# Kernel optimization log

Measured on AMD Instinct MI355X. Metric: run time of the kernel, lower is better.

## Reference

```python
import jax, jax.numpy as jnp
import numpy as np

CORE_DIM = 128
MEMORY_SLOTS = 64
B, S = 4, 4096


def setup_inputs() -> dict:
    key = jax.random.key(0)
    k1, k2, k3, k4, k5 = jax.random.split(key, 5)
    x = jax.random.normal(k1, (B, S, CORE_DIM), dtype=jnp.float32)
    memory_keys = jax.random.normal(k2, (MEMORY_SLOTS, CORE_DIM), dtype=jnp.float32)
    memory_ops = jax.random.normal(k3, (MEMORY_SLOTS, CORE_DIM, CORE_DIM), dtype=jnp.float32)
    # nn.Linear(core_dim, core_dim): weight [out, in], bias [out]
    bound = 1.0 / np.sqrt(CORE_DIM)
    Wq = jax.random.uniform(k4, (CORE_DIM, CORE_DIM), minval=-bound, maxval=bound, dtype=jnp.float32)
    bq = jax.random.uniform(k5, (CORE_DIM,), minval=-bound, maxval=bound, dtype=jnp.float32)
    return {"input_tensor": x, "memory_keys": memory_keys, "memory_ops": memory_ops, "Wq": Wq, "bq": bq}


def reference(input_tensor, memory_keys, memory_ops, Wq, bq):
    dim = input_tensor.shape[-1]
    # query projection: x @ Wq^T + bq
    queries = jnp.einsum('bsd,ed->bse', input_tensor, Wq) + bq
    # soft attention over memory slots
    attn_logits = jnp.einsum('bsd,md->bsm', queries, memory_keys)
    attn_weights = jax.nn.softmax(attn_logits / jnp.sqrt(jnp.float32(dim)), axis=-1)
    # fused: (sum_m attn[bsm] * ops[m]) @ x[bs]  == sum_m attn[bsm] * (ops[m] @ x[bs])
    processed = jnp.einsum('bsm,mde,bse->bsd', attn_weights, memory_ops, input_tensor)
    return processed
```

## Files before the change

kernel.cpp:

```cpp
#include <hip/hip_runtime.h>

typedef __bf16 bf16x8 __attribute__((ext_vector_type(8)));
typedef float f32x4 __attribute__((ext_vector_type(4)));
typedef unsigned int uint4v __attribute__((ext_vector_type(4)));
typedef unsigned short ushort_t;
typedef unsigned int uint_t;

#define RS 0.08838834764831845f

__device__ __forceinline__ ushort_t f2bf(float f) {
    uint_t u = __float_as_uint(f);
    u += 0x7FFFu + ((u >> 16) & 1u);
    return (ushort_t)(u >> 16);
}
__device__ __forceinline__ uint_t pack2(float a, float b) {
    return (uint_t)f2bf(a) | ((uint_t)f2bf(b) << 16);
}
union U4B8 { uint4v u; bf16x8 b; };
__device__ __forceinline__ bf16x8 as_bf(uint4v u) { U4B8 x; x.u = u; return x.b; }

__device__ __forceinline__ int xfrag(int f, int lane) {
    return f * 1072 + ((lane >> 4) * 272) + ((lane & 15) * 16);
}

__device__ __forceinline__ void gload16(const void* g, void* l) {
    __builtin_amdgcn_global_load_lds(
        (const __attribute__((address_space(1))) void*)g,
        (__attribute__((address_space(3))) void*)l, 16, 0, 0);
}

__global__ __launch_bounds__(256) void prep_kernel(
    const float* __restrict__ ops, const float* __restrict__ keys,
    const float* __restrict__ Wq, const float* __restrict__ bq,
    uint4v* __restrict__ ops_sw, ushort_t* __restrict__ kp_sw,
    float* __restrict__ cb)
{
    const int tid = threadIdx.x;
    const int b = blockIdx.x;
    if (b >= 64) {
        int g = (b - 64) * 256 + tid;
        int L = g & 63, dt = (g >> 6) & 7, ks = (g >> 9) & 3, m = g >> 11;
        int d = dt * 16 + (L & 15);
        int e0 = ks * 32 + ((L >> 4) << 3);
        const float4* s = (const float4*)(ops + (((size_t)(m * 128 + d)) << 7) + e0);
        float4 v0 = s[0], v1 = s[1];
        uint4v o = { pack2(v0.x, v0.y), pack2(v0.z, v0.w),
                     pack2(v1.x, v1.y), pack2(v1.z, v1.w) };
        int h = m * 2048 + (dt >> 2) * 1024 + ks * 256 + (dt & 3) * 64 + L;
        ops_sw[h] = o;
    } else {
        __shared__ float red[256];
        const int m = b;
        const int d = tid & 127, eh = tid >> 7;
        const float* kr = keys + m * 128 + eh * 64;
        const float* wc = Wq + (size_t)(eh * 64) * 128 + d;
        float acc = 0.f;
        #pragma unroll 8
        for (int e = 0; e < 64; ++e)
            acc = fmaf(kr[e], wc[(size_t)e * 128], acc);
        red[tid] = acc;
        __syncthreads();
        if (tid < 128) {
            float v = red[tid] + red[tid + 128];
            int ki = d >> 5, qq = (d >> 3) & 3, j = d & 7;
            kp_sw[((((ki * 4 + (m >> 4)) * 64) + (qq * 16 + (m & 15))) << 3) | j] = f2bf(v);
        } else if (tid >= 192) {
            int lane = tid - 192;
            float p = keys[m * 128 + lane] * bq[lane]
                    + keys[m * 128 + 64 + lane] * bq[64 + lane];
            #pragma unroll
            for (int off = 1; off < 64; off <<= 1) p += __shfl_xor(p, off);
            if (lane == 0) cb[m] = p;
        }
    }
}

__global__ __launch_bounds__(512, 2) void main_kernel(
    const float* __restrict__ x, const float* __restrict__ cb,
    const ushort_t* __restrict__ kp_sw, const uint4v* __restrict__ ops_sw,
    float* __restrict__ out)
{
    __shared__ __align__(16) unsigned char lds[132096];
    float* attn_f = (float*)lds;
    unsigned char* xs = lds + 33792;
    uint4v* bb = (uint4v*)(lds + 33792);

    const int tid = threadIdx.x;
    const int lane = tid & 63;
    const int w = tid >> 6;
    const int q = lane >> 4;
    const int l15 = lane & 15;
    const int tb = blockIdx.x >> 1;
    const int dh = blockIdx.x & 1;
    const int t0 = tb * 128;
    const int dtp = w & 3;
    const int tg = w >> 2;

    {
        const float4* x4 = (const float4*)(x + (size_t)t0 * 128);
        #pragma unroll
        for (int it = 0; it < 4; ++it) {
            int i = it * 512 + tid;
            int t = i >> 4, kc = i & 15;
            float4 a = x4[t * 32 + kc * 2];
            float4 b2 = x4[t * 32 + kc * 2 + 1];
            uint4v o = { pack2(a.x, a.y), pack2(a.z, a.w),
                         pack2(b2.x, b2.y), pack2(b2.z, b2.w) };
            *(uint4v*)(xs + ((t >> 4) * 4 + (kc >> 2)) * 1072
                          + (kc & 3) * 272 + (t & 15) * 16) = o;
        }
    }
    __syncthreads();

    {
        f32x4 L0 = {0,0,0,0}, L1 = {0,0,0,0}, L2 = {0,0,0,0}, L3 = {0,0,0,0};
        const uint4v* kpf = (const uint4v*)kp_sw;
        #pragma unroll
        for (int ki = 0; ki < 4; ++ki) {
            bf16x8 a = *(const bf16x8*)(xs + xfrag(w * 4 + ki, lane));
            L0 = __builtin_amdgcn_mfma_f32_16x16x32_bf16(a, as_bf(kpf[(ki*4+0)*64 + lane]), L0, 0,0,0);
            L1 = __builtin_amdgcn_mfma_f32_16x16x32_bf16(a, as_bf(kpf[(ki*4+1)*64 + lane]), L1, 0,0,0);
            L2 = __builtin_amdgcn_mfma_f32_16x16x32_bf16(a, as_bf(kpf[(ki*4+2)*64 + lane]), L2, 0,0,0);
            L3 = __builtin_amdgcn_mfma_f32_16x16x32_bf16(a, as_bf(kpf[(ki*4+3)*64 + lane]), L3, 0,0,0);
        }
        float c0 = cb[l15], c1 = cb[16 + l15], c2 = cb[32 + l15], c3 = cb[48 + l15];
        #pragma unroll
        for (int r = 0; r < 4; ++r) {
            float v0 = (L0[r] + c0) * RS;
            float v1 = (L1[r] + c1) * RS;
            float v2 = (L2[r] + c2) * RS;
            float v3 = (L3[r] + c3) * RS;
            float mx = fmaxf(fmaxf(v0, v1), fmaxf(v2, v3));
            #pragma unroll
            for (int off = 1; off < 16; off <<= 1) mx = fmaxf(mx, __shfl_xor(mx, off));
            float e0 = __expf(v0 - mx), e1 = __expf(v1 - mx),
                  e2 = __expf(v2 - mx), e3 = __expf(v3 - mx);
            float sm = e0 + e1 + e2 + e3;
            #pragma unroll
            for (int off = 1; off < 16; off <<= 1) sm += __shfl_xor(sm, off);
            float inv = 1.0f / sm;
            int t = w * 16 + q * 4 + r;
            attn_f[(     l15) * 132 + t] = e0 * inv;
            attn_f[(16 + l15) * 132 + t] = e1 * inv;
            attn_f[(32 + l15) * 132 + t] = e2 * inv;
            attn_f[(48 + l15) * 132 + t] = e3 * inv;
        }
    }

    bf16x8 A[4][4];
    #pragma unroll
    for (int tf = 0; tf < 4; ++tf)
        #pragma unroll
        for (int ki = 0; ki < 4; ++ki)
            A[tf][ki] = *(const bf16x8*)(xs + xfrag(tg * 16 + tf * 4 + ki, lane));

    __syncthreads();

    auto stage = [&](int pair, int b) {
        uint4v* dst = bb + b * 2048 + w * 64;
        const uint4v* src = ops_sw + (size_t)pair * 4096 + dh * 1024 + w * 64 + lane;
        #pragma unroll
        for (int j = 0; j < 4; ++j) {
            const uint4v* g = src + (j >> 1) * 2048 + (j & 1) * 512;
            gload16((const void*)g, (void*)(dst + j * 512));
        }
    };

    f32x4 C[4] = {};

    auto computePair = [&](int p) {
        const uint4v* bbuf = bb + (p % 3) * 2048 + dtp * 64 + lane;
        #pragma unroll
        for (int sl = 0; sl < 2; ++sl) {
            const int m = p * 2 + sl;
            f32x4 S[4] = {};
            __builtin_amdgcn_s_setprio(1);
            #pragma unroll
            for (int ki = 0; ki < 4; ++ki) {
                bf16x8 bfrag = as_bf(bbuf[sl * 1024 + ki * 256]);
                #pragma unroll
                for (int tf = 0; tf < 4; ++tf)
                    S[tf] = __builtin_amdgcn_mfma_f32_16x16x32_bf16(A[tf][ki], bfrag, S[tf], 0,0,0);
            }
            __builtin_amdgcn_s_setprio(0);
            #pragma unroll
            for (int tf = 0; tf < 4; ++tf) {
                f32x4 af = *(const f32x4*)&attn_f[m * 132 + tg * 64 + tf * 16 + q * 4];
                #pragma unroll
                for (int r = 0; r < 4; ++r)
                    C[tf][r] = fmaf(af[r], S[tf][r], C[tf][r]);
            }
        }
    };

    stage(0, 0);
    for (int p = 0; p < 31; ++p) {
        stage(p + 1, (p + 1) % 3);
        asm volatile("s_waitcnt vmcnt(4)" ::: "memory");
        __builtin_amdgcn_s_barrier();
        computePair(p);
    }
    asm volatile("s_waitcnt vmcnt(0)" ::: "memory");
    __builtin_amdgcn_s_barrier();
    computePair(31);

    float* op = out + (size_t)t0 * 128 + dh * 64 + dtp * 16 + l15;
    #pragma unroll
    for (int tf = 0; tf < 4; ++tf)
        #pragma unroll
        for (int r = 0; r < 4; ++r)
            op[(size_t)(tg * 64 + tf * 16 + q * 4 + r) * 128] = C[tf][r];
}

extern "C" void kernel_launch(void* const* d_in, const int* in_sizes, int n_in,
                              void* d_out, int out_size, void* d_ws, size_t ws_size,
                              hipStream_t stream)
{
    const float* x    = (const float*)d_in[0];
    const float* keys = (const float*)d_in[1];
    const float* ops  = (const float*)d_in[2];
    const float* Wq   = (const float*)d_in[3];
    const float* bq   = (const float*)d_in[4];
    float* out = (float*)d_out;

    char* ws = (char*)d_ws;
    uint4v*   ops_sw = (uint4v*)ws;
    ushort_t* kp_sw  = (ushort_t*)(ws + 2097152);
    float*    cb     = (float*)(ws + 2097152 + 16384);

    prep_kernel<<<576, 256, 0, stream>>>(ops, keys, Wq, bq, ops_sw, kp_sw, cb);
    main_kernel<<<256, 512, 0, stream>>>(x, cb, kp_sw, ops_sw, out);
}
```

Baseline: 104.7 us.

## Fuse prep into main kernel with a grid-wide atomic barrier

Merges the weight-preparation kernel into the main kernel. Every block converts its share of the memory ops to bf16, and the first 64 blocks compute the projected keys and bias terms. A device-wide atomic counter barrier then waits for all 256 blocks before the attention and contraction phases, and the first ops stage is issued before the logits computation. This removes a kernel launch and the gap between the two kernels, but adds a memset launch and a spin barrier that requires all blocks to be co-resident. It also removes the attn row padding, which may introduce LDS bank conflicts.

```diff
diff --git a/kernel.cpp b/kernel.cpp
--- a/kernel.cpp
+++ b/kernel.cpp
@@ -29,61 +29,19 @@
         (__attribute__((address_space(3))) void*)l, 16, 0, 0);
 }
 
-__global__ __launch_bounds__(256) void prep_kernel(
-    const float* __restrict__ ops, const float* __restrict__ keys,
-    const float* __restrict__ Wq, const float* __restrict__ bq,
+__global__ __launch_bounds__(512, 2) void fused_kernel(
+    const float* __restrict__ x, const float* __restrict__ keys,
+    const float* __restrict__ ops, const float* __restrict__ Wq,
+    const float* __restrict__ bq,
     uint4v* __restrict__ ops_sw, ushort_t* __restrict__ kp_sw,
-    float* __restrict__ cb)
-{
-    const int tid = threadIdx.x;
-    const int b = blockIdx.x;
-    if (b >= 64) {
-        int g = (b - 64) * 256 + tid;
-        int L = g & 63, dt = (g >> 6) & 7, ks = (g >> 9) & 3, m = g >> 11;
-        int d = dt * 16 + (L & 15);
-        int e0 = ks * 32 + ((L >> 4) << 3);
-        const float4* s = (const float4*)(ops + (((size_t)(m * 128 + d)) << 7) + e0);
-        float4 v0 = s[0], v1 = s[1];
-        uint4v o = { pack2(v0.x, v0.y), pack2(v0.z, v0.w),
-                     pack2(v1.x, v1.y), pack2(v1.z, v1.w) };
-        int h = m * 2048 + (dt >> 2) * 1024 + ks * 256 + (dt & 3) * 64 + L;
-        ops_sw[h] = o;
-    } else {
-        __shared__ float red[256];
-        const int m = b;
-        const int d = tid & 127, eh = tid >> 7;
-        const float* kr = keys + m * 128 + eh * 64;
-        const float* wc = Wq + (size_t)(eh * 64) * 128 + d;
-        float acc = 0.f;
-        #pragma unroll 8
-        for (int e = 0; e < 64; ++e)
-            acc = fmaf(kr[e], wc[(size_t)e * 128], acc);
-        red[tid] = acc;
-        __syncthreads();
-        if (tid < 128) {
-            float v = red[tid] + red[tid + 128];
-            int ki = d >> 5, qq = (d >> 3) & 3, j = d & 7;
-            kp_sw[((((ki * 4 + (m >> 4)) * 64) + (qq * 16 + (m & 15))) << 3) | j] = f2bf(v);
-        } else if (tid >= 192) {
-            int lane = tid - 192;
-            float p = keys[m * 128 + lane] * bq[lane]
-                    + keys[m * 128 + 64 + lane] * bq[64 + lane];
-            #pragma unroll
-            for (int off = 1; off < 64; off <<= 1) p += __shfl_xor(p, off);
-            if (lane == 0) cb[m] = p;
-        }
-    }
-}
-
-__global__ __launch_bounds__(512, 2) void main_kernel(
-    const float* __restrict__ x, const float* __restrict__ cb,
-    const ushort_t* __restrict__ kp_sw, const uint4v* __restrict__ ops_sw,
+    float* __restrict__ cb, unsigned int* __restrict__ cnt,
     float* __restrict__ out)
 {
-    __shared__ __align__(16) unsigned char lds[132096];
+    __shared__ __align__(16) unsigned char lds[131072];
     float* attn_f = (float*)lds;
-    unsigned char* xs = lds + 33792;
-    uint4v* bb = (uint4v*)(lds + 33792);
+    uint4v* bb = (uint4v*)(lds + 32768);
+    unsigned char* xs = lds + 65536;
+    float* red = (float*)(lds + 129024);
 
     const int tid = threadIdx.x;
     const int lane = tid & 63;
@@ -97,6 +55,44 @@
     const int tg = w >> 2;
 
     {
+        int g = blockIdx.x * 512 + tid;
+        int L = g & 63, dt = (g >> 6) & 7, ks = (g >> 9) & 3, m = g >> 11;
+        int d = dt * 16 + (L & 15);
+        int e0 = ks * 32 + ((L >> 4) << 3);
+        const float4* s = (const float4*)(ops + (((size_t)(m * 128 + d)) << 7) + e0);
+        float4 v0 = s[0], v1 = s[1];
+        uint4v o = { pack2(v0.x, v0.y), pack2(v0.z, v0.w),
+                     pack2(v1.x, v1.y), pack2(v1.z, v1.w) };
+        int h = m * 2048 + (dt >> 2) * 1024 + ks * 256 + (dt & 3) * 64 + L;
+        ops_sw[h] = o;
+    }
+
+    if (blockIdx.x < 64) {
+        const int m = blockIdx.x;
+        const int d = tid & 127, eh = tid >> 7;
+        const float* kr = keys + m * 128 + eh * 32;
+        const float* wc = Wq + (size_t)(eh * 32) * 128 + d;
+        float acc = 0.f;
+        #pragma unroll 8
+        for (int e = 0; e < 32; ++e)
+            acc = fmaf(kr[e], wc[(size_t)e * 128], acc);
+        red[tid] = acc;
+        __syncthreads();
+        if (tid < 128) {
+            float v = red[tid] + red[tid + 128] + red[tid + 256] + red[tid + 384];
+            int ki = d >> 5, qq = (d >> 3) & 3, j = d & 7;
+            kp_sw[((((ki * 4 + (m >> 4)) * 64) + (qq * 16 + (m & 15))) << 3) | j] = f2bf(v);
+        } else if (tid >= 448) {
+            int lane2 = tid - 448;
+            float pv = keys[m * 128 + lane2] * bq[lane2]
+                     + keys[m * 128 + 64 + lane2] * bq[64 + lane2];
+            #pragma unroll
+            for (int off = 1; off < 64; off <<= 1) pv += __shfl_xor(pv, off);
+            if (lane2 == 0) cb[m] = pv;
+        }
+    }
+
+    {
         const float4* x4 = (const float4*)(x + (size_t)t0 * 128);
         #pragma unroll
         for (int it = 0; it < 4; ++it) {
@@ -110,7 +106,27 @@
                           + (kc & 3) * 272 + (t & 15) * 16) = o;
         }
     }
+
     __syncthreads();
+    __threadfence();
+    if (tid == 0) {
+        __hip_atomic_fetch_add(cnt, 1u, __ATOMIC_RELEASE, __HIP_MEMORY_SCOPE_AGENT);
+        while (__hip_atomic_load(cnt, __ATOMIC_RELAXED, __HIP_MEMORY_SCOPE_AGENT) < 256u) {}
+        __builtin_amdgcn_fence(__ATOMIC_ACQUIRE, "agent");
+    }
+    __syncthreads();
+
+    auto stage = [&](int pair, int b) {
+        uint4v* dst = bb + b * 2048 + w * 64;
+        const uint4v* src = ops_sw + (size_t)pair * 4096 + dh * 1024 + w * 64 + lane;
+        #pragma unroll
+        for (int j = 0; j < 4; ++j) {
+            const uint4v* g = src + (j >> 1) * 2048 + (j & 1) * 512;
+            gload16((const void*)g, (void*)(dst + j * 512));
+        }
+    };
+
+    stage(0, 0);
 
     {
         f32x4 L0 = {0,0,0,0}, L1 = {0,0,0,0}, L2 = {0,0,0,0}, L3 = {0,0,0,0};
@@ -140,10 +156,10 @@
             for (int off = 1; off < 16; off <<= 1) sm += __shfl_xor(sm, off);
             float inv = 1.0f / sm;
             int t = w * 16 + q * 4 + r;
-            attn_f[(     l15) * 132 + t] = e0 * inv;
-            attn_f[(16 + l15) * 132 + t] = e1 * inv;
-            attn_f[(32 + l15) * 132 + t] = e2 * inv;
-            attn_f[(48 + l15) * 132 + t] = e3 * inv;
+            attn_f[(     l15) * 128 + t] = e0 * inv;
+            attn_f[(16 + l15) * 128 + t] = e1 * inv;
+            attn_f[(32 + l15) * 128 + t] = e2 * inv;
+            attn_f[(48 + l15) * 128 + t] = e3 * inv;
         }
     }
 
@@ -155,16 +171,6 @@
             A[tf][ki] = *(const bf16x8*)(xs + xfrag(tg * 16 + tf * 4 + ki, lane));
 
     __syncthreads();
-
-    auto stage = [&](int pair, int b) {
-        uint4v* dst = bb + b * 2048 + w * 64;
-        const uint4v* src = ops_sw + (size_t)pair * 4096 + dh * 1024 + w * 64 + lane;
-        #pragma unroll
-        for (int j = 0; j < 4; ++j) {
-            const uint4v* g = src + (j >> 1) * 2048 + (j & 1) * 512;
-            gload16((const void*)g, (void*)(dst + j * 512));
-        }
-    };
 
     f32x4 C[4] = {};
 
@@ -185,7 +191,7 @@
             __builtin_amdgcn_s_setprio(0);
             #pragma unroll
             for (int tf = 0; tf < 4; ++tf) {
-                f32x4 af = *(const f32x4*)&attn_f[m * 132 + tg * 64 + tf * 16 + q * 4];
+                f32x4 af = *(const f32x4*)&attn_f[m * 128 + tg * 64 + tf * 16 + q * 4];
                 #pragma unroll
                 for (int r = 0; r < 4; ++r)
                     C[tf][r] = fmaf(af[r], S[tf][r], C[tf][r]);
@@ -193,7 +199,6 @@
         }
     };
 
-    stage(0, 0);
     for (int p = 0; p < 31; ++p) {
         stage(p + 1, (p + 1) % 3);
         asm volatile("s_waitcnt vmcnt(4)" ::: "memory");
@@ -224,10 +229,12 @@
     float* out = (float*)d_out;
 
     char* ws = (char*)d_ws;
-    uint4v*   ops_sw = (uint4v*)ws;
-    ushort_t* kp_sw  = (ushort_t*)(ws + 2097152);
-    float*    cb     = (float*)(ws + 2097152 + 16384);
-
-    prep_kernel<<<576, 256, 0, stream>>>(ops, keys, Wq, bq, ops_sw, kp_sw, cb);
-    main_kernel<<<256, 512, 0, stream>>>(x, cb, kp_sw, ops_sw, out);
-}
+    uint4v*       ops_sw = (uint4v*)ws;
+    ushort_t*     kp_sw  = (ushort_t*)(ws + 2097152);
+    float*        cb     = (float*)(ws + 2097152 + 16384);
+    unsigned int* cnt    = (unsigned int*)(ws + 2097152 + 16384 + 256);
+
+    hipMemsetAsync((void*)cnt, 0, 64, stream);
+    fused_kernel<<<256, 512, 0, stream>>>(x, keys, ops, Wq, bq,
+                                          ops_sw, kp_sw, cb, cnt, out);
+}
```

Measured after the change: 155.3 us. 48.3% more time.

## Register double-buffer B fragments, overlap first ops stage with softmax, swizzle attn LDS

Applied to the files above, without the earlier changes.

The ops staging buffer now has its own LDS region, separate from the attention and x regions, so the first global-to-LDS stage is issued before the logits/softmax phase and overlaps with it. The main loop is unrolled by two and keeps two register sets of B fragments: the next pair is read from LDS while the MFMAs for the current pair run. The attention matrix drops its padded stride of 132 for a stride of 128 with an XOR swizzle to avoid bank conflicts. In exchange, register pressure rises by 32 VGPRs, which at launch bounds (512,2) could cause spills.

```diff
diff --git a/kernel.cpp b/kernel.cpp
--- a/kernel.cpp
+++ b/kernel.cpp
@@ -80,10 +80,10 @@
     const ushort_t* __restrict__ kp_sw, const uint4v* __restrict__ ops_sw,
     float* __restrict__ out)
 {
-    __shared__ __align__(16) unsigned char lds[132096];
-    float* attn_f = (float*)lds;
-    unsigned char* xs = lds + 33792;
-    uint4v* bb = (uint4v*)(lds + 33792);
+    __shared__ __align__(16) unsigned char lds[131072];
+    uint4v* bb = (uint4v*)lds;
+    unsigned char* xs = lds + 32768;
+    float* attn_f = (float*)(lds + 98304);
 
     const int tid = threadIdx.x;
     const int lane = tid & 63;
@@ -96,6 +96,16 @@
     const int dtp = w & 3;
     const int tg = w >> 2;
 
+    auto stage = [&](int pair, int b) {
+        uint4v* dst = bb + b * 2048 + w * 64;
+        const uint4v* src = ops_sw + (size_t)pair * 4096 + dh * 1024 + w * 64 + lane;
+        #pragma unroll
+        for (int j = 0; j < 4; ++j) {
+            const uint4v* g = src + (j >> 1) * 2048 + (j & 1) * 512;
+            gload16((const void*)g, (void*)(dst + j * 512));
+        }
+    };
+
     {
         const float4* x4 = (const float4*)(x + (size_t)t0 * 128);
         #pragma unroll
@@ -112,6 +122,8 @@
     }
     __syncthreads();
 
+    stage(0, 0);
+
     {
         f32x4 L0 = {0,0,0,0}, L1 = {0,0,0,0}, L2 = {0,0,0,0}, L3 = {0,0,0,0};
         const uint4v* kpf = (const uint4v*)kp_sw;
@@ -140,10 +152,11 @@
             for (int off = 1; off < 16; off <<= 1) sm += __shfl_xor(sm, off);
             float inv = 1.0f / sm;
             int t = w * 16 + q * 4 + r;
-            attn_f[(     l15) * 132 + t] = e0 * inv;
-            attn_f[(16 + l15) * 132 + t] = e1 * inv;
-            attn_f[(32 + l15) * 132 + t] = e2 * inv;
-            attn_f[(48 + l15) * 132 + t] = e3 * inv;
+            int ts = t ^ ((l15 & 7) << 2);
+            attn_f[(     l15) * 128 + ts] = e0 * inv;
+            attn_f[(16 + l15) * 128 + ts] = e1 * inv;
+            attn_f[(32 + l15) * 128 + ts] = e2 * inv;
+            attn_f[(48 + l15) * 128 + ts] = e3 * inv;
         }
     }
 
@@ -156,36 +169,37 @@
 
     __syncthreads();
 
-    auto stage = [&](int pair, int b) {
-        uint4v* dst = bb + b * 2048 + w * 64;
-        const uint4v* src = ops_sw + (size_t)pair * 4096 + dh * 1024 + w * 64 + lane;
-        #pragma unroll
-        for (int j = 0; j < 4; ++j) {
-            const uint4v* g = src + (j >> 1) * 2048 + (j & 1) * 512;
-            gload16((const void*)g, (void*)(dst + j * 512));
-        }
+    f32x4 C[4] = {};
+    uint4v RA[2][4], RB[2][4];
+
+    auto loadPair = [&](int k, uint4v (&R)[2][4]) {
+        const uint4v* bbuf = bb + (k % 3) * 2048 + dtp * 64 + lane;
+        #pragma unroll
+        for (int sl = 0; sl < 2; ++sl)
+            #pragma unroll
+            for (int ki = 0; ki < 4; ++ki)
+                R[sl][ki] = bbuf[sl * 1024 + ki * 256];
     };
 
-    f32x4 C[4] = {};
-
-    auto computePair = [&](int p) {
-        const uint4v* bbuf = bb + (p % 3) * 2048 + dtp * 64 + lane;
+    auto mfmaPair = [&](int k, uint4v (&R)[2][4]) {
         #pragma unroll
         for (int sl = 0; sl < 2; ++sl) {
-            const int m = p * 2 + sl;
+            const int m = 2 * k + sl;
+            const int msw = (m & 7) << 2;
             f32x4 S[4] = {};
             __builtin_amdgcn_s_setprio(1);
             #pragma unroll
             for (int ki = 0; ki < 4; ++ki) {
-                bf16x8 bfrag = as_bf(bbuf[sl * 1024 + ki * 256]);
+                bf16x8 bf = as_bf(R[sl][ki]);
                 #pragma unroll
                 for (int tf = 0; tf < 4; ++tf)
-                    S[tf] = __builtin_amdgcn_mfma_f32_16x16x32_bf16(A[tf][ki], bfrag, S[tf], 0,0,0);
+                    S[tf] = __builtin_amdgcn_mfma_f32_16x16x32_bf16(A[tf][ki], bf, S[tf], 0,0,0);
             }
             __builtin_amdgcn_s_setprio(0);
             #pragma unroll
             for (int tf = 0; tf < 4; ++tf) {
-                f32x4 af = *(const f32x4*)&attn_f[m * 132 + tg * 64 + tf * 16 + q * 4];
+                int ta = (tg * 64 + tf * 16 + q * 4) ^ msw;
+                f32x4 af = *(const f32x4*)&attn_f[m * 128 + ta];
                 #pragma unroll
                 for (int r = 0; r < 4; ++r)
                     C[tf][r] = fmaf(af[r], S[tf][r], C[tf][r]);
@@ -193,16 +207,30 @@
         }
     };
 
-    stage(0, 0);
-    for (int p = 0; p < 31; ++p) {
-        stage(p + 1, (p + 1) % 3);
+    stage(1, 1);
+    asm volatile("s_waitcnt vmcnt(4)" ::: "memory");
+    __builtin_amdgcn_s_barrier();
+    loadPair(0, RA);
+
+    #pragma unroll 1
+    for (int k = 1; k < 31; k += 2) {
+        stage(k + 1, (k + 1) % 3);
         asm volatile("s_waitcnt vmcnt(4)" ::: "memory");
         __builtin_amdgcn_s_barrier();
-        computePair(p);
+        loadPair(k, RB);
+        mfmaPair(k - 1, RA);
+
+        stage(k + 2, (k + 2) % 3);
+        asm volatile("s_waitcnt vmcnt(4)" ::: "memory");
+        __builtin_amdgcn_s_barrier();
+        loadPair(k + 1, RA);
+        mfmaPair(k, RB);
     }
     asm volatile("s_waitcnt vmcnt(0)" ::: "memory");
     __builtin_amdgcn_s_barrier();
-    computePair(31);
+    loadPair(31, RB);
+    mfmaPair(30, RA);
+    mfmaPair(31, RB);
 
     float* op = out + (size_t)t0 * 128 + dh * 64 + dtp * 16 + l15;
     #pragma unroll
```

Result: no change. 105.2 us (+0.5%).

## Split memory slots across waves and reduce partial outputs through LDS

Applied to the files above, without the earlier changes.

Warps are now split by slot parity instead of by token half. Each warp loads its B fragments once per slot and reuses them across all 128 tokens, with the partial sums reduced through LDS at the end. The LDS layout is rearranged so the attention buffer no longer aliases the ops staging buffers, and it uses an XOR swizzle in place of padding. The first ops stage is also issued before the softmax so it overlaps with it. The cost is twice the A fragments and accumulators held in registers per thread, which may hurt occupancy or cause spills, plus an extra reduction pass.

```diff
diff --git a/kernel.cpp b/kernel.cpp
--- a/kernel.cpp
+++ b/kernel.cpp
@@ -80,10 +80,10 @@
     const ushort_t* __restrict__ kp_sw, const uint4v* __restrict__ ops_sw,
     float* __restrict__ out)
 {
-    __shared__ __align__(16) unsigned char lds[132096];
-    float* attn_f = (float*)lds;
-    unsigned char* xs = lds + 33792;
-    uint4v* bb = (uint4v*)(lds + 33792);
+    __shared__ __align__(16) unsigned char lds[131072];
+    uint4v* bb = (uint4v*)lds;
+    unsigned char* xs = lds + 32768;
+    float* attn_f = (float*)(lds + 98304);
 
     const int tid = threadIdx.x;
     const int lane = tid & 63;
@@ -93,8 +93,18 @@
     const int tb = blockIdx.x >> 1;
     const int dh = blockIdx.x & 1;
     const int t0 = tb * 128;
-    const int dtp = w & 3;
-    const int tg = w >> 2;
+    const int slh = w & 1;
+    const int dtp = w >> 1;
+
+    auto stage = [&](int pair, int b) {
+        uint4v* dst = bb + b * 2048 + w * 64;
+        const uint4v* src = ops_sw + (size_t)pair * 4096 + dh * 1024 + w * 64 + lane;
+        #pragma unroll
+        for (int j = 0; j < 4; ++j) {
+            const uint4v* g = src + (j >> 1) * 2048 + (j & 1) * 512;
+            gload16((const void*)g, (void*)(dst + j * 512));
+        }
+    };
 
     {
         const float4* x4 = (const float4*)(x + (size_t)t0 * 128);
@@ -112,6 +122,8 @@
     }
     __syncthreads();
 
+    stage(0, 0);
+
     {
         f32x4 L0 = {0,0,0,0}, L1 = {0,0,0,0}, L2 = {0,0,0,0}, L3 = {0,0,0,0};
         const uint4v* kpf = (const uint4v*)kp_sw;
@@ -140,60 +152,54 @@
             for (int off = 1; off < 16; off <<= 1) sm += __shfl_xor(sm, off);
             float inv = 1.0f / sm;
             int t = w * 16 + q * 4 + r;
-            attn_f[(     l15) * 132 + t] = e0 * inv;
-            attn_f[(16 + l15) * 132 + t] = e1 * inv;
-            attn_f[(32 + l15) * 132 + t] = e2 * inv;
-            attn_f[(48 + l15) * 132 + t] = e3 * inv;
-        }
-    }
-
-    bf16x8 A[4][4];
+            int ts = t ^ ((l15 & 7) << 2);
+            attn_f[(     l15) * 128 + ts] = e0 * inv;
+            attn_f[(16 + l15) * 128 + ts] = e1 * inv;
+            attn_f[(32 + l15) * 128 + ts] = e2 * inv;
+            attn_f[(48 + l15) * 128 + ts] = e3 * inv;
+        }
+    }
+
+    bf16x8 A[8][4];
     #pragma unroll
-    for (int tf = 0; tf < 4; ++tf)
+    for (int tf = 0; tf < 8; ++tf)
         #pragma unroll
         for (int ki = 0; ki < 4; ++ki)
-            A[tf][ki] = *(const bf16x8*)(xs + xfrag(tg * 16 + tf * 4 + ki, lane));
-
-    __syncthreads();
-
-    auto stage = [&](int pair, int b) {
-        uint4v* dst = bb + b * 2048 + w * 64;
-        const uint4v* src = ops_sw + (size_t)pair * 4096 + dh * 1024 + w * 64 + lane;
-        #pragma unroll
-        for (int j = 0; j < 4; ++j) {
-            const uint4v* g = src + (j >> 1) * 2048 + (j & 1) * 512;
-            gload16((const void*)g, (void*)(dst + j * 512));
-        }
-    };
-
-    f32x4 C[4] = {};
+            A[tf][ki] = *(const bf16x8*)(xs + xfrag(tf * 4 + ki, lane));
+
+    __syncthreads();
+
+    f32x4 C[8] = {};
 
     auto computePair = [&](int p) {
-        const uint4v* bbuf = bb + (p % 3) * 2048 + dtp * 64 + lane;
-        #pragma unroll
-        for (int sl = 0; sl < 2; ++sl) {
-            const int m = p * 2 + sl;
+        const uint4v* bbuf = bb + (p % 3) * 2048 + slh * 1024 + dtp * 64 + lane;
+        const int m = 2 * p + slh;
+        const int msw = (m & 7) << 2;
+        bf16x8 Bf[4];
+        #pragma unroll
+        for (int ki = 0; ki < 4; ++ki) Bf[ki] = as_bf(bbuf[ki * 256]);
+        #pragma unroll
+        for (int th = 0; th < 2; ++th) {
             f32x4 S[4] = {};
             __builtin_amdgcn_s_setprio(1);
             #pragma unroll
-            for (int ki = 0; ki < 4; ++ki) {
-                bf16x8 bfrag = as_bf(bbuf[sl * 1024 + ki * 256]);
+            for (int ki = 0; ki < 4; ++ki)
                 #pragma unroll
                 for (int tf = 0; tf < 4; ++tf)
-                    S[tf] = __builtin_amdgcn_mfma_f32_16x16x32_bf16(A[tf][ki], bfrag, S[tf], 0,0,0);
-            }
+                    S[tf] = __builtin_amdgcn_mfma_f32_16x16x32_bf16(
+                        A[th * 4 + tf][ki], Bf[ki], S[tf], 0, 0, 0);
             __builtin_amdgcn_s_setprio(0);
             #pragma unroll
             for (int tf = 0; tf < 4; ++tf) {
-                f32x4 af = *(const f32x4*)&attn_f[m * 132 + tg * 64 + tf * 16 + q * 4];
+                int ta = ((th * 4 + tf) * 16 + q * 4) ^ msw;
+                f32x4 af = *(const f32x4*)&attn_f[m * 128 + ta];
                 #pragma unroll
                 for (int r = 0; r < 4; ++r)
-                    C[tf][r] = fmaf(af[r], S[tf][r], C[tf][r]);
+                    C[th * 4 + tf][r] = fmaf(af[r], S[tf][r], C[th * 4 + tf][r]);
             }
         }
     };
 
-    stage(0, 0);
     for (int p = 0; p < 31; ++p) {
         stage(p + 1, (p + 1) % 3);
         asm volatile("s_waitcnt vmcnt(4)" ::: "memory");
@@ -204,12 +210,24 @@
     __builtin_amdgcn_s_barrier();
     computePair(31);
 
-    float* op = out + (size_t)t0 * 128 + dh * 64 + dtp * 16 + l15;
-    #pragma unroll
-    for (int tf = 0; tf < 4; ++tf)
-        #pragma unroll
-        for (int r = 0; r < 4; ++r)
-            op[(size_t)(tg * 64 + tf * 16 + q * 4 + r) * 128] = C[tf][r];
+    __syncthreads();
+    f32x4* rb = (f32x4*)(lds + 98304);
+    if (slh == 1) {
+        #pragma unroll
+        for (int tf = 0; tf < 8; ++tf)
+            rb[dtp * 512 + tf * 64 + lane] = C[tf];
+    }
+    __syncthreads();
+    if (slh == 0) {
+        float* op = out + (size_t)t0 * 128 + dh * 64 + dtp * 16 + l15;
+        #pragma unroll
+        for (int tf = 0; tf < 8; ++tf) {
+            f32x4 other = rb[dtp * 512 + tf * 64 + lane];
+            #pragma unroll
+            for (int r = 0; r < 4; ++r)
+                op[(size_t)(tf * 16 + q * 4 + r) * 128] = C[tf][r] + other[r];
+        }
+    }
 }
 
 extern "C" void kernel_launch(void* const* d_in, const int* in_sizes, int n_in,
```

Result: slower. 108.2 us (+3.3%).
